# Kernel tuning notes

Hardware: AMD Instinct MI355X
Metric: run time of the kernel (lower is better)

## Reference

```python
import jax, jax.numpy as jnp
import numpy as np

N_USERS = 100000
N_MOVIES = 50000
EMB_DIM = 64
N_EDGES = 5000000


def setup_inputs() -> dict:
    key = jax.random.key(0)
    k1, k2, k3 = jax.random.split(key, 3)
    N = N_USERS + N_MOVIES
    edge_index = jax.random.randint(k1, (2, N_EDGES), 0, N, dtype=jnp.int64)
    user_emb = 0.1 * jax.random.normal(k2, (N_USERS, EMB_DIM), dtype=jnp.float32)
    movie_emb = 0.1 * jax.random.normal(k3, (N_MOVIES, EMB_DIM), dtype=jnp.float32)
    return {"edge_index": edge_index, "n_layers": 3,
            "user_emb": user_emb, "movie_emb": movie_emb}


def reference(edge_index, n_layers, user_emb, movie_emb):
    n_users = user_emb.shape[0]
    N = n_users + movie_emb.shape[0]
    x = jnp.concatenate([user_emb, movie_emb], axis=0)  # [N, D]

    row, col = edge_index[0], edge_index[1]  # source -> target
    # gcn_norm without self-loops (LGConv default): deg from target (col)
    deg = jnp.zeros((N,), x.dtype).at[col].add(1.0)
    dis = jnp.where(deg > 0, jax.lax.rsqrt(jnp.maximum(deg, 1.0)), 0.0)
    norm = dis[row] * dis[col]  # [E]

    acc = x
    total = x
    for _ in range(n_layers):
        msg = acc[row] * norm[:, None]            # [E, D] gather + scale
        acc = jax.ops.segment_sum(msg, col, num_segments=N)  # scatter-add
        total = total + acc
    final = total / (n_layers + 1)                # mean over layers 0..K
    return final[:n_users], final[n_users:]
```

## Files before the change

kernel.cpp:

```cpp
#include <hip/hip_runtime.h>

typedef _Float16 half_t;
typedef _Float16 half2_t __attribute__((ext_vector_type(2)));
union pk_u { unsigned int u; half2_t h; };

#define EMB 64
#define NLAYERS 3
#define BSH2 8
#define BW2 256
#define NB2MAX 1024
#define GSPREAD 32
#define SUBC 8
#define CAP 10240
#define SUBCAP 1280
#define EGCAP 16384
#define P1_BATCH 8192
#define P1_TH 1024
#define P1_EPT 8
#define BINTH 512

__device__ inline int wave_incl_scan(int v) {
    #pragma unroll
    for (int off = 1; off < 64; off <<= 1) {
        int u = __shfl_up(v, off);
        if ((threadIdx.x & 63) >= off) v += u;
    }
    return v;
}

__device__ inline void scan1024(const int* __restrict__ in, int* __restrict__ lstart,
                                int* __restrict__ wsum) {
    int t = threadIdx.x;
    int orig = in[t];
    int v = wave_incl_scan(orig);
    if ((t & 63) == 63) wsum[t >> 6] = v;
    __syncthreads();
    int wid = t >> 6;
    int base = 0;
    #pragma unroll
    for (int w = 0; w < 15; ++w) base += (w < wid) ? wsum[w] : 0;
    lstart[t] = base + v - orig;
    __syncthreads();
}

__device__ inline void scan256(const int* __restrict__ in, int* __restrict__ lstart,
                               int* __restrict__ wsum) {
    int t = threadIdx.x;
    int v = 0, orig = 0;
    if (t < 256) {
        orig = in[t];
        v = wave_incl_scan(orig);
        if ((t & 63) == 63) wsum[t >> 6] = v;
    }
    __syncthreads();
    if (t < 256) {
        int wid = t >> 6;
        int base = 0;
        #pragma unroll
        for (int w = 0; w < 3; ++w) base += (w < wid) ? wsum[w] : 0;
        lstart[t] = base + v - orig;
    }
    __syncthreads();
}

__global__ __launch_bounds__(1024) void part_kernel(
        const int* __restrict__ row, const int* __restrict__ col,
        int* __restrict__ gcount, int* __restrict__ tmp, int E, int nb2) {
    __shared__ int hist[NB2MAX];
    __shared__ int lstart[NB2MAX];
    __shared__ int gbase[NB2MAX];
    __shared__ int wsum[16];
    __shared__ int srec[P1_BATCH];
    __shared__ unsigned short sbuck[P1_BATCH];

    int base = blockIdx.x * P1_BATCH;
    int nE = min(P1_BATCH, E - base);
    int s = blockIdx.x & (SUBC - 1);

    if (threadIdx.x < NB2MAX) hist[threadIdx.x] = 0;
    __syncthreads();

    int myc[P1_EPT];
    #pragma unroll
    for (int k = 0; k < P1_EPT; ++k) {
        int idx = base + (k << 10) + threadIdx.x;
        int c = (idx < E) ? col[idx] : -1;
        myc[k] = c;
        if (c >= 0) atomicAdd(&hist[c >> BSH2], 1);
    }
    __syncthreads();

    scan1024(hist, lstart, wsum);

    if (threadIdx.x < nb2) {
        int b = threadIdx.x;
        int c = hist[b];
        int off = 0;
        if (c > 0) off = atomicAdd(&gcount[(s * NB2MAX + b) * GSPREAD], c);
        gbase[b] = b * CAP + s * SUBCAP + off - lstart[b];
    }
    __syncthreads();
    if (threadIdx.x < NB2MAX) hist[threadIdx.x] = lstart[threadIdx.x];
    __syncthreads();

    #pragma unroll
    for (int k = 0; k < P1_EPT; ++k) {
        int idx = base + (k << 10) + threadIdx.x;
        if (idx < E) {
            int c = myc[k];
            int b = c >> BSH2;
            int r = row[idx];
            int pos = atomicAdd(&hist[b], 1);
            srec[pos] = (r << BSH2) | (c & (BW2 - 1));
            sbuck[pos] = (unsigned short)b;
        }
    }
    __syncthreads();

    if (nE == P1_BATCH) {
        #pragma unroll
        for (int k = 0; k < P1_BATCH / P1_TH; ++k) {
            int i = (k << 10) + threadIdx.x;
            tmp[gbase[sbuck[i]] + i] = srec[i];
        }
    } else {
        for (int i = threadIdx.x; i < nE; i += P1_TH)
            tmp[gbase[sbuck[i]] + i] = srec[i];
    }
}

__global__ __launch_bounds__(512) void bin_kernel(
        const int* __restrict__ tmp, const int* __restrict__ gcount,
        int* __restrict__ eg, int2* __restrict__ sd, float* __restrict__ dis,
        const float4* __restrict__ uev, const float4* __restrict__ mev,
        uint2* __restrict__ s0v, uint2* __restrict__ sbz,
        int n_users, int N) {
    __shared__ int srec[CAP];
    __shared__ int hist[BW2];
    __shared__ int padh[BW2];
    __shared__ int lstart[BW2];
    __shared__ int wsum[4];
    __shared__ float sdis[BW2];
    int b = blockIdx.x;
    int rbase = b * CAP;
    int ebase = b * EGCAP;
    int c0 = b << BSH2;
    int nc = min(BW2, N - c0);
    int sent = N << 7;

    for (int i = threadIdx.x; i < BW2; i += BINTH) hist[i] = 0;
    __syncthreads();

    int cnt = 0;
    #pragma unroll
    for (int ss = 0; ss < SUBC; ++ss) {
        int cs = gcount[(ss * NB2MAX + b) * GSPREAD];
        int sb = rbase + ss * SUBCAP;
        for (int i = threadIdx.x; i < cs; i += BINTH) {
            int rec = tmp[sb + i];
            srec[cnt + i] = rec;
            atomicAdd(&hist[rec & (BW2 - 1)], 1);
        }
        cnt += cs;
    }
    __syncthreads();

    for (int c = threadIdx.x; c < BW2; c += BINTH)
        padh[c] = (hist[c] + 31) & ~31;
    __syncthreads();

    scan256(padh, lstart, wsum);

    for (int c = threadIdx.x; c < nc; c += BINTH) {
        int d = hist[c];
        float dn = (d > 0) ? rsqrtf((float)d) : 0.0f;
        sd[c0 + c] = make_int2(ebase + lstart[c], padh[c]);
        dis[c0 + c] = dn;
        sdis[c] = dn;
    }
    __syncthreads();
    for (int i = threadIdx.x; i < BW2; i += BINTH) hist[i] = lstart[i];
    __syncthreads();

    for (int i = threadIdx.x; i < cnt; i += BINTH) {
        int v = srec[i];
        int pos = atomicAdd(&hist[v & (BW2 - 1)], 1);
        eg[ebase + pos] = (v >> BSH2) << 7;
    }
    __syncthreads();

    for (int i = threadIdx.x; i < BW2 * 32; i += BINTH) {
        int c = i >> 5;
        int o = i & 31;
        int st = hist[c];
        int en = lstart[c] + padh[c];
        if (st + o < en) eg[ebase + st + o] = sent;
    }
    int tot = lstart[BW2 - 1] + padh[BW2 - 1];
    if (threadIdx.x < 64) eg[ebase + tot + threadIdx.x] = sent;

    if (b == 0 && threadIdx.x < 32) {
        int q = threadIdx.x & 15;
        uint2 z = make_uint2(0u, 0u);
        if (threadIdx.x < 16) s0v[(long long)N * 16 + q] = z;
        else                  sbz[(long long)N * 16 + q] = z;
    }

    for (int i = threadIdx.x; i < nc * 16; i += BINTH) {
        int loc = i >> 4;
        int node = c0 + loc;
        int q = i & 15;
        const float4* src = (node < n_users) ? (uev + (long long)node * 16)
                                             : (mev + (long long)(node - n_users) * 16);
        float4 v = src[q];
        float dn = sdis[loc];
        pk_u w0, w1;
        w0.h[0] = (half_t)(v.x * dn); w0.h[1] = (half_t)(v.y * dn);
        w1.h[0] = (half_t)(v.z * dn); w1.h[1] = (half_t)(v.w * dn);
        s0v[(long long)node * 16 + q] = make_uint2(w0.u, w1.u);
    }
}

template <int LAYER>
__global__ __launch_bounds__(256) void gather_kernel(
        const int* __restrict__ eg, const int2* __restrict__ sd,
        const float* __restrict__ dis,
        const uint4* __restrict__ tab, uint2* __restrict__ sOut,
        const uint2* __restrict__ s1v, const uint2* __restrict__ s2v,
        const float4* __restrict__ uev, const float4* __restrict__ mev,
        float4* __restrict__ outv, int n_users, int N) {
    int wave = blockIdx.x * (blockDim.x >> 6) + (threadIdx.x >> 6);
    if (wave >= N) return;
    int l = threadIdx.x & 63;
    int p = l & 7;
    int h = l >> 3;
    unsigned pb = (unsigned)p << 4;
    const char* tb = (const char*)tab;

    int2 se = sd[wave];
    int j = se.x;
    int e = se.x + se.y;
    pk_u a0, a1, a2, a3;
    a0.u = 0; a1.u = 0; a2.u = 0; a3.u = 0;

    if (j < e) {
        int r0 = eg[j + h];
        int r1 = eg[j + 8 + h];
        int r2 = eg[j + 16 + h];
        int r3 = eg[j + 24 + h];
        for (; j < e; j += 32) {
            int n0 = eg[j + 32 + h];
            int n1 = eg[j + 40 + h];
            int n2 = eg[j + 48 + h];
            int n3 = eg[j + 56 + h];
            uint4 v0 = *(const uint4*)(tb + ((unsigned)r0 + pb));
            uint4 v1 = *(const uint4*)(tb + ((unsigned)r1 + pb));
            uint4 v2 = *(const uint4*)(tb + ((unsigned)r2 + pb));
            uint4 v3 = *(const uint4*)(tb + ((unsigned)r3 + pb));
            pk_u t;
            t.u = v0.x; a0.h += t.h; t.u = v0.y; a1.h += t.h;
            t.u = v0.z; a2.h += t.h; t.u = v0.w; a3.h += t.h;
            t.u = v1.x; a0.h += t.h; t.u = v1.y; a1.h += t.h;
            t.u = v1.z; a2.h += t.h; t.u = v1.w; a3.h += t.h;
            t.u = v2.x; a0.h += t.h; t.u = v2.y; a1.h += t.h;
            t.u = v2.z; a2.h += t.h; t.u = v2.w; a3.h += t.h;
            t.u = v3.x; a0.h += t.h; t.u = v3.y; a1.h += t.h;
            t.u = v3.z; a2.h += t.h; t.u = v3.w; a3.h += t.h;
            r0 = n0; r1 = n1; r2 = n2; r3 = n3;
        }
    }

    #pragma unroll
    for (int m = 8; m <= 32; m <<= 1) {
        pk_u t;
        t.u = (unsigned int)__shfl_xor((int)a0.u, m); a0.h += t.h;
        t.u = (unsigned int)__shfl_xor((int)a1.u, m); a1.h += t.h;
        t.u = (unsigned int)__shfl_xor((int)a2.u, m); a2.h += t.h;
        t.u = (unsigned int)__shfl_xor((int)a3.u, m); a3.h += t.h;
    }

    if (h < 2) {
        pk_u x0 = h ? a2 : a0;
        pk_u x1 = h ? a3 : a1;
        float dc = dis[wave];
        float g0 = dc * (float)x0.h[0];
        float g1 = dc * (float)x0.h[1];
        float g2 = dc * (float)x1.h[0];
        float g3 = dc * (float)x1.h[1];
        int q = p * 2 + h;
        long long o16 = (long long)wave * 16 + q;
        if (LAYER < 3) {
            pk_u w0, w1;
            w0.h[0] = (half_t)(dc * g0); w0.h[1] = (half_t)(dc * g1);
            w1.h[0] = (half_t)(dc * g2); w1.h[1] = (half_t)(dc * g3);
            sOut[o16] = make_uint2(w0.u, w1.u);
        } else {
            const float4* src = (wave < n_users) ? (uev + (long long)wave * 16)
                                                 : (mev + (long long)(wave - n_users) * 16);
            float4 xv = src[q];
            float inv = (dc > 0.0f) ? (1.0f / dc) : 0.0f;
            uint2 sa2 = s1v[o16];
            uint2 sb2 = s2v[o16];
            pk_u pa, pb2, pc, pd;
            pa.u = sa2.x; pb2.u = sa2.y; pc.u = sb2.x; pd.u = sb2.y;
            float4 r;
            r.x = (xv.x + ((float)pa.h[0]  + (float)pc.h[0]) * inv + g0) * 0.25f;
            r.y = (xv.y + ((float)pa.h[1]  + (float)pc.h[1]) * inv + g1) * 0.25f;
            r.z = (xv.z + ((float)pb2.h[0] + (float)pd.h[0]) * inv + g2) * 0.25f;
            r.w = (xv.w + ((float)pb2.h[1] + (float)pd.h[1]) * inv + g3) * 0.25f;
            outv[o16] = r;
        }
    }
}

extern "C" void kernel_launch(void* const* d_in, const int* in_sizes, int n_in,
                              void* d_out, int out_size, void* d_ws, size_t ws_size,
                              hipStream_t stream) {
    const int*   edge = (const int*)d_in[0];
    const float* ue   = (const float*)d_in[2];
    const float* me   = (const float*)d_in[3];
    float*       out  = (float*)d_out;

    const int E        = in_sizes[0] / 2;
    const int n_users  = in_sizes[2] / EMB;
    const int n_movies = in_sizes[3] / EMB;
    const int N        = n_users + n_movies;
    const int* row = edge;
    const int* col = edge + E;
    const int nb2 = (N + BW2 - 1) >> BSH2;

    char* ws = (char*)d_ws;
    auto align_up = [](size_t v) { return (v + 255) & ~(size_t)255; };
    int*    gcount = (int*)ws;    ws += align_up((size_t)NB2MAX * SUBC * GSPREAD * sizeof(int));
    int2*   sd     = (int2*)ws;   ws += align_up((size_t)N * sizeof(int2));
    float*  dis    = (float*)ws;  ws += align_up((size_t)N * sizeof(float));
    int*    tmp    = (int*)ws;    ws += align_up((size_t)nb2 * CAP * sizeof(int));
    int*    eg     = (int*)ws;    ws += align_up((size_t)nb2 * EGCAP * sizeof(int));
    half_t* sA     = (half_t*)ws; ws += align_up((size_t)(N + 1) * EMB * sizeof(half_t));
    half_t* sB     = (half_t*)ws; ws += align_up((size_t)(N + 1) * EMB * sizeof(half_t));

    hipMemsetAsync(gcount, 0, (size_t)NB2MAX * SUBC * GSPREAD * sizeof(int), stream);
    part_kernel<<<(E + P1_BATCH - 1) / P1_BATCH, P1_TH, 0, stream>>>(
        row, col, gcount, tmp, E, nb2);
    bin_kernel<<<nb2, BINTH, 0, stream>>>(
        tmp, gcount, eg, sd, dis,
        (const float4*)ue, (const float4*)me, (uint2*)sA, (uint2*)sB,
        n_users, N);

    const int waves_per_block = 4;
    const int gblocks = (N + waves_per_block - 1) / waves_per_block;
    gather_kernel<1><<<gblocks, 256, 0, stream>>>(
        eg, sd, dis, (const uint4*)sA, (uint2*)sB,
        nullptr, nullptr, nullptr, nullptr, nullptr, n_users, N);
    gather_kernel<2><<<gblocks, 256, 0, stream>>>(
        eg, sd, dis, (const uint4*)sB, (uint2*)sA,
        nullptr, nullptr, nullptr, nullptr, nullptr, n_users, N);
    gather_kernel<3><<<gblocks, 256, 0, stream>>>(
        eg, sd, dis, (const uint4*)sA, nullptr,
        (const uint2*)sB, (const uint2*)sA,
        (const float4*)ue, (const float4*)me, (float4*)out, n_users, N);
}
```

Measured before the change: 444.2 us.

## Split bin kernel into two half-bucket blocks and stage edge image in LDS

Each 256-node bucket is now handled by two blocks, each filtering the records for its 128-node half. This doubles grid parallelism and cuts per-block LDS needs. The sorted edge list and its sentinel padding are built in shared memory and then copied out with coalesced int4 stores, replacing scattered global writes. The cost is that every record is read twice across the two blocks. There is also a truncation risk if a half-bucket exceeds SRECMAX or EGIMG.

```diff
diff --git a/kernel.cpp b/kernel.cpp
--- a/kernel.cpp
+++ b/kernel.cpp
@@ -8,12 +8,15 @@
 #define NLAYERS 3
 #define BSH2 8
 #define BW2 256
+#define HB 128
 #define NB2MAX 1024
 #define GSPREAD 32
 #define SUBC 8
 #define CAP 10240
 #define SUBCAP 1280
-#define EGCAP 16384
+#define SRECMAX 5376
+#define EGIMG 9408
+#define EGCAP EGIMG
 #define P1_BATCH 8192
 #define P1_TH 1024
 #define P1_EPT 8
@@ -43,21 +46,18 @@
     __syncthreads();
 }
 
-__device__ inline void scan256(const int* __restrict__ in, int* __restrict__ lstart,
+__device__ inline void scan128(const int* __restrict__ in, int* __restrict__ lstart,
                                int* __restrict__ wsum) {
     int t = threadIdx.x;
     int v = 0, orig = 0;
-    if (t < 256) {
+    if (t < 128) {
         orig = in[t];
         v = wave_incl_scan(orig);
         if ((t & 63) == 63) wsum[t >> 6] = v;
     }
     __syncthreads();
-    if (t < 256) {
-        int wid = t >> 6;
-        int base = 0;
-        #pragma unroll
-        for (int w = 0; w < 3; ++w) base += (w < wid) ? wsum[w] : 0;
+    if (t < 128) {
+        int base = (t >= 64) ? wsum[0] : 0;
         lstart[t] = base + v - orig;
     }
     __syncthreads();
@@ -135,71 +135,87 @@
         const float4* __restrict__ uev, const float4* __restrict__ mev,
         uint2* __restrict__ s0v, uint2* __restrict__ sbz,
         int n_users, int N) {
-    __shared__ int srec[CAP];
-    __shared__ int hist[BW2];
-    __shared__ int padh[BW2];
-    __shared__ int lstart[BW2];
-    __shared__ int wsum[4];
-    __shared__ float sdis[BW2];
-    int b = blockIdx.x;
+    __shared__ alignas(16) int egl[EGIMG];
+    __shared__ int srec[SRECMAX];
+    __shared__ int hist[HB];
+    __shared__ int padh[HB];
+    __shared__ int lstart[HB];
+    __shared__ int curs[HB];
+    __shared__ int wsum[2];
+    __shared__ float sdis[HB];
+    __shared__ int nselS;
+
+    int g = blockIdx.x;
+    int b = g >> 1;
+    int h = g & 1;
     int rbase = b * CAP;
-    int ebase = b * EGCAP;
-    int c0 = b << BSH2;
-    int nc = min(BW2, N - c0);
+    int ebase = g * EGCAP;
+    int c0 = (b << BSH2) + (h << 7);
+    int nc = min(HB, N - c0);
     int sent = N << 7;
 
-    for (int i = threadIdx.x; i < BW2; i += BINTH) hist[i] = 0;
-    __syncthreads();
-
-    int cnt = 0;
+    if (threadIdx.x < HB) hist[threadIdx.x] = 0;
+    if (threadIdx.x == 0) nselS = 0;
+    __syncthreads();
+
     #pragma unroll
     for (int ss = 0; ss < SUBC; ++ss) {
         int cs = gcount[(ss * NB2MAX + b) * GSPREAD];
         int sb = rbase + ss * SUBCAP;
         for (int i = threadIdx.x; i < cs; i += BINTH) {
             int rec = tmp[sb + i];
-            srec[cnt + i] = rec;
-            atomicAdd(&hist[rec & (BW2 - 1)], 1);
-        }
-        cnt += cs;
-    }
-    __syncthreads();
-
-    for (int c = threadIdx.x; c < BW2; c += BINTH)
-        padh[c] = (hist[c] + 31) & ~31;
-    __syncthreads();
-
-    scan256(padh, lstart, wsum);
-
-    for (int c = threadIdx.x; c < nc; c += BINTH) {
-        int d = hist[c];
-        float dn = (d > 0) ? rsqrtf((float)d) : 0.0f;
-        sd[c0 + c] = make_int2(ebase + lstart[c], padh[c]);
-        dis[c0 + c] = dn;
-        sdis[c] = dn;
-    }
-    __syncthreads();
-    for (int i = threadIdx.x; i < BW2; i += BINTH) hist[i] = lstart[i];
-    __syncthreads();
-
-    for (int i = threadIdx.x; i < cnt; i += BINTH) {
+            if (((rec >> 7) & 1) == h) {
+                int pos = atomicAdd(&nselS, 1);
+                if (pos < SRECMAX) srec[pos] = rec;
+                atomicAdd(&hist[rec & (HB - 1)], 1);
+            }
+        }
+    }
+    __syncthreads();
+    int nsel = min(nselS, SRECMAX);
+
+    if (threadIdx.x < HB) padh[threadIdx.x] = (hist[threadIdx.x] + 31) & ~31;
+    __syncthreads();
+
+    scan128(padh, lstart, wsum);
+
+    if (threadIdx.x < HB) {
+        int c = threadIdx.x;
+        if (c < nc) {
+            int d = hist[c];
+            float dn = (d > 0) ? rsqrtf((float)d) : 0.0f;
+            sd[c0 + c] = make_int2(ebase + lstart[c], padh[c]);
+            dis[c0 + c] = dn;
+            sdis[c] = dn;
+        }
+        curs[c] = lstart[c];
+    }
+    __syncthreads();
+
+    for (int i = threadIdx.x; i < nsel; i += BINTH) {
         int v = srec[i];
-        int pos = atomicAdd(&hist[v & (BW2 - 1)], 1);
-        eg[ebase + pos] = (v >> BSH2) << 7;
-    }
-    __syncthreads();
-
-    for (int i = threadIdx.x; i < BW2 * 32; i += BINTH) {
+        int pos = atomicAdd(&curs[v & (HB - 1)], 1);
+        egl[pos] = (v >> 1) & ~127;
+    }
+    __syncthreads();
+
+    for (int i = threadIdx.x; i < HB * 32; i += BINTH) {
         int c = i >> 5;
         int o = i & 31;
-        int st = hist[c];
+        int st = lstart[c] + hist[c];
         int en = lstart[c] + padh[c];
-        if (st + o < en) eg[ebase + st + o] = sent;
-    }
-    int tot = lstart[BW2 - 1] + padh[BW2 - 1];
-    if (threadIdx.x < 64) eg[ebase + tot + threadIdx.x] = sent;
-
-    if (b == 0 && threadIdx.x < 32) {
+        if (st + o < en) egl[st + o] = sent;
+    }
+    int tot = lstart[HB - 1] + padh[HB - 1];
+    if (threadIdx.x < 64) egl[tot + threadIdx.x] = sent;
+    __syncthreads();
+
+    int tw = (tot + 64) >> 2;
+    int4* dst = (int4*)(eg + ebase);
+    const int4* srci = (const int4*)egl;
+    for (int i = threadIdx.x; i < tw; i += BINTH) dst[i] = srci[i];
+
+    if (g == 0 && threadIdx.x < 32) {
         int q = threadIdx.x & 15;
         uint2 z = make_uint2(0u, 0u);
         if (threadIdx.x < 16) s0v[(long long)N * 16 + q] = z;
@@ -335,14 +351,14 @@
     int2*   sd     = (int2*)ws;   ws += align_up((size_t)N * sizeof(int2));
     float*  dis    = (float*)ws;  ws += align_up((size_t)N * sizeof(float));
     int*    tmp    = (int*)ws;    ws += align_up((size_t)nb2 * CAP * sizeof(int));
-    int*    eg     = (int*)ws;    ws += align_up((size_t)nb2 * EGCAP * sizeof(int));
+    int*    eg     = (int*)ws;    ws += align_up((size_t)nb2 * 2 * EGCAP * sizeof(int));
     half_t* sA     = (half_t*)ws; ws += align_up((size_t)(N + 1) * EMB * sizeof(half_t));
     half_t* sB     = (half_t*)ws; ws += align_up((size_t)(N + 1) * EMB * sizeof(half_t));
 
     hipMemsetAsync(gcount, 0, (size_t)NB2MAX * SUBC * GSPREAD * sizeof(int), stream);
     part_kernel<<<(E + P1_BATCH - 1) / P1_BATCH, P1_TH, 0, stream>>>(
         row, col, gcount, tmp, E, nb2);
-    bin_kernel<<<nb2, BINTH, 0, stream>>>(
+    bin_kernel<<<2 * nb2, BINTH, 0, stream>>>(
         tmp, gcount, eg, sd, dis,
         (const float4*)ue, (const float4*)me, (uint2*)sA, (uint2*)sB,
         n_users, N);
```

After: 443.4 us. About the same (-0.2%).

## Replace two-pass bucket partition with global histogram, scan, and atomic scatter CSR build

Applied to the files above, without the earlier changes.

Replaces the bucketed two-level partition (part_kernel plus bin_kernel with shared-memory staging) with a classic CSR build. A per-node global histogram is split over 8 sub-planes, then a two-level prefix scan, a finalize pass that sets offsets, padding and scaled fp16 embeddings, and an atomic scatter of rows into the edge list. This removes the bounded-capacity bucket buffers and the intermediate tmp copy. In exchange it uses global atomics on per-node counters and fully random scatter writes, and the order of edges within a node becomes nondeterministic.

```diff
diff --git a/kernel.cpp b/kernel.cpp
--- a/kernel.cpp
+++ b/kernel.cpp
@@ -6,18 +6,9 @@
 
 #define EMB 64
 #define NLAYERS 3
-#define BSH2 8
-#define BW2 256
-#define NB2MAX 1024
-#define GSPREAD 32
 #define SUBC 8
-#define CAP 10240
-#define SUBCAP 1280
-#define EGCAP 16384
-#define P1_BATCH 8192
-#define P1_TH 1024
-#define P1_EPT 8
-#define BINTH 512
+#define EBLK 8192
+#define NBLK 1024
 
 __device__ inline int wave_incl_scan(int v) {
     #pragma unroll
@@ -28,196 +19,129 @@
     return v;
 }
 
-__device__ inline void scan1024(const int* __restrict__ in, int* __restrict__ lstart,
-                                int* __restrict__ wsum) {
+__global__ __launch_bounds__(1024) void hist_kernel(
+        const int* __restrict__ col, int* __restrict__ cnt2, int E, int NPAD) {
+    int base = blockIdx.x * EBLK;
+    int s = blockIdx.x & (SUBC - 1);
+    int* plane = cnt2 + s * NPAD;
+    #pragma unroll
+    for (int k = 0; k < 8; ++k) {
+        int idx = base + (k << 10) + threadIdx.x;
+        if (idx < E) atomicAdd(&plane[col[idx]], 1);
+    }
+}
+
+__global__ __launch_bounds__(1024) void scanA_kernel(
+        const int* __restrict__ cnt2, int* __restrict__ lstartG,
+        int* __restrict__ bsum, int N, int NPAD) {
+    __shared__ int wsum[16];
+    int node = blockIdx.x * NBLK + threadIdx.x;
+    int pt = 0;
+    if (node < N) {
+        int deg = 0;
+        #pragma unroll
+        for (int s = 0; s < SUBC; ++s) deg += cnt2[s * NPAD + node];
+        pt = (deg + 31) & ~31;
+    }
+    int v = wave_incl_scan(pt);
+    if ((threadIdx.x & 63) == 63) wsum[threadIdx.x >> 6] = v;
+    __syncthreads();
+    int wid = threadIdx.x >> 6;
+    int base = 0;
+    #pragma unroll
+    for (int w = 0; w < 15; ++w) base += (w < wid) ? wsum[w] : 0;
+    if (node < N) lstartG[node] = base + v - pt;
+    if (threadIdx.x == 1023) bsum[blockIdx.x] = base + v;
+}
+
+__global__ __launch_bounds__(1024) void scanB_kernel(
+        const int* __restrict__ bsum, int* __restrict__ bbase,
+        int* __restrict__ totalG, int nb) {
+    __shared__ int wsum[16];
     int t = threadIdx.x;
-    int orig = in[t];
-    int v = wave_incl_scan(orig);
+    int v0 = (t < nb) ? bsum[t] : 0;
+    int v = wave_incl_scan(v0);
     if ((t & 63) == 63) wsum[t >> 6] = v;
     __syncthreads();
     int wid = t >> 6;
     int base = 0;
     #pragma unroll
     for (int w = 0; w < 15; ++w) base += (w < wid) ? wsum[w] : 0;
-    lstart[t] = base + v - orig;
-    __syncthreads();
-}
-
-__device__ inline void scan256(const int* __restrict__ in, int* __restrict__ lstart,
-                               int* __restrict__ wsum) {
-    int t = threadIdx.x;
-    int v = 0, orig = 0;
-    if (t < 256) {
-        orig = in[t];
-        v = wave_incl_scan(orig);
-        if ((t & 63) == 63) wsum[t >> 6] = v;
-    }
-    __syncthreads();
-    if (t < 256) {
-        int wid = t >> 6;
-        int base = 0;
-        #pragma unroll
-        for (int w = 0; w < 3; ++w) base += (w < wid) ? wsum[w] : 0;
-        lstart[t] = base + v - orig;
-    }
-    __syncthreads();
-}
-
-__global__ __launch_bounds__(1024) void part_kernel(
-        const int* __restrict__ row, const int* __restrict__ col,
-        int* __restrict__ gcount, int* __restrict__ tmp, int E, int nb2) {
-    __shared__ int hist[NB2MAX];
-    __shared__ int lstart[NB2MAX];
-    __shared__ int gbase[NB2MAX];
-    __shared__ int wsum[16];
-    __shared__ int srec[P1_BATCH];
-    __shared__ unsigned short sbuck[P1_BATCH];
-
-    int base = blockIdx.x * P1_BATCH;
-    int nE = min(P1_BATCH, E - base);
-    int s = blockIdx.x & (SUBC - 1);
-
-    if (threadIdx.x < NB2MAX) hist[threadIdx.x] = 0;
-    __syncthreads();
-
-    int myc[P1_EPT];
-    #pragma unroll
-    for (int k = 0; k < P1_EPT; ++k) {
-        int idx = base + (k << 10) + threadIdx.x;
-        int c = (idx < E) ? col[idx] : -1;
-        myc[k] = c;
-        if (c >= 0) atomicAdd(&hist[c >> BSH2], 1);
-    }
-    __syncthreads();
-
-    scan1024(hist, lstart, wsum);
-
-    if (threadIdx.x < nb2) {
-        int b = threadIdx.x;
-        int c = hist[b];
-        int off = 0;
-        if (c > 0) off = atomicAdd(&gcount[(s * NB2MAX + b) * GSPREAD], c);
-        gbase[b] = b * CAP + s * SUBCAP + off - lstart[b];
-    }
-    __syncthreads();
-    if (threadIdx.x < NB2MAX) hist[threadIdx.x] = lstart[threadIdx.x];
-    __syncthreads();
-
-    #pragma unroll
-    for (int k = 0; k < P1_EPT; ++k) {
-        int idx = base + (k << 10) + threadIdx.x;
-        if (idx < E) {
-            int c = myc[k];
-            int b = c >> BSH2;
-            int r = row[idx];
-            int pos = atomicAdd(&hist[b], 1);
-            srec[pos] = (r << BSH2) | (c & (BW2 - 1));
-            sbuck[pos] = (unsigned short)b;
-        }
-    }
-    __syncthreads();
-
-    if (nE == P1_BATCH) {
-        #pragma unroll
-        for (int k = 0; k < P1_BATCH / P1_TH; ++k) {
-            int i = (k << 10) + threadIdx.x;
-            tmp[gbase[sbuck[i]] + i] = srec[i];
-        }
-    } else {
-        for (int i = threadIdx.x; i < nE; i += P1_TH)
-            tmp[gbase[sbuck[i]] + i] = srec[i];
-    }
-}
-
-__global__ __launch_bounds__(512) void bin_kernel(
-        const int* __restrict__ tmp, const int* __restrict__ gcount,
+    if (t < nb) bbase[t] = base + v - v0;
+    if (t == 1023) *totalG = base + v;
+}
+
+__global__ __launch_bounds__(1024) void finalize_kernel(
+        int* __restrict__ cnt2, const int* __restrict__ lstartG,
+        const int* __restrict__ bbase, const int* __restrict__ totalG,
         int* __restrict__ eg, int2* __restrict__ sd, float* __restrict__ dis,
         const float4* __restrict__ uev, const float4* __restrict__ mev,
         uint2* __restrict__ s0v, uint2* __restrict__ sbz,
-        int n_users, int N) {
-    __shared__ int srec[CAP];
-    __shared__ int hist[BW2];
-    __shared__ int padh[BW2];
-    __shared__ int lstart[BW2];
-    __shared__ int wsum[4];
-    __shared__ float sdis[BW2];
-    int b = blockIdx.x;
-    int rbase = b * CAP;
-    int ebase = b * EGCAP;
-    int c0 = b << BSH2;
-    int nc = min(BW2, N - c0);
+        int n_users, int N, int NPAD) {
+    __shared__ float sdis[NBLK];
+    int c0 = blockIdx.x * NBLK;
+    int node = c0 + threadIdx.x;
     int sent = N << 7;
 
-    for (int i = threadIdx.x; i < BW2; i += BINTH) hist[i] = 0;
+    if (node < N) {
+        int c[SUBC];
+        int deg = 0;
+        #pragma unroll
+        for (int s = 0; s < SUBC; ++s) { c[s] = cnt2[s * NPAD + node]; deg += c[s]; }
+        int pt = (deg + 31) & ~31;
+        int start = bbase[blockIdx.x] + lstartG[node];
+        float dn = (deg > 0) ? rsqrtf((float)deg) : 0.0f;
+        sd[node] = make_int2(start, pt);
+        dis[node] = dn;
+        sdis[threadIdx.x] = dn;
+        int off = start;
+        #pragma unroll
+        for (int s = 0; s < SUBC; ++s) { int cc = c[s]; cnt2[s * NPAD + node] = off; off += cc; }
+        for (int k = start + deg; k < start + pt; ++k) eg[k] = sent;
+        if (node == N - 1) {
+            int tot = *totalG;
+            for (int k = 0; k < 64; ++k) eg[tot + k] = sent;
+            for (int q = 0; q < 16; ++q) {
+                s0v[(long long)N * 16 + q] = make_uint2(0u, 0u);
+                sbz[(long long)N * 16 + q] = make_uint2(0u, 0u);
+            }
+        }
+    } else {
+        sdis[threadIdx.x] = 0.0f;
+    }
     __syncthreads();
 
-    int cnt = 0;
-    #pragma unroll
-    for (int ss = 0; ss < SUBC; ++ss) {
-        int cs = gcount[(ss * NB2MAX + b) * GSPREAD];
-        int sb = rbase + ss * SUBCAP;
-        for (int i = threadIdx.x; i < cs; i += BINTH) {
-            int rec = tmp[sb + i];
-            srec[cnt + i] = rec;
-            atomicAdd(&hist[rec & (BW2 - 1)], 1);
-        }
-        cnt += cs;
-    }
-    __syncthreads();
-
-    for (int c = threadIdx.x; c < BW2; c += BINTH)
-        padh[c] = (hist[c] + 31) & ~31;
-    __syncthreads();
-
-    scan256(padh, lstart, wsum);
-
-    for (int c = threadIdx.x; c < nc; c += BINTH) {
-        int d = hist[c];
-        float dn = (d > 0) ? rsqrtf((float)d) : 0.0f;
-        sd[c0 + c] = make_int2(ebase + lstart[c], padh[c]);
-        dis[c0 + c] = dn;
-        sdis[c] = dn;
-    }
-    __syncthreads();
-    for (int i = threadIdx.x; i < BW2; i += BINTH) hist[i] = lstart[i];
-    __syncthreads();
-
-    for (int i = threadIdx.x; i < cnt; i += BINTH) {
-        int v = srec[i];
-        int pos = atomicAdd(&hist[v & (BW2 - 1)], 1);
-        eg[ebase + pos] = (v >> BSH2) << 7;
-    }
-    __syncthreads();
-
-    for (int i = threadIdx.x; i < BW2 * 32; i += BINTH) {
-        int c = i >> 5;
-        int o = i & 31;
-        int st = hist[c];
-        int en = lstart[c] + padh[c];
-        if (st + o < en) eg[ebase + st + o] = sent;
-    }
-    int tot = lstart[BW2 - 1] + padh[BW2 - 1];
-    if (threadIdx.x < 64) eg[ebase + tot + threadIdx.x] = sent;
-
-    if (b == 0 && threadIdx.x < 32) {
-        int q = threadIdx.x & 15;
-        uint2 z = make_uint2(0u, 0u);
-        if (threadIdx.x < 16) s0v[(long long)N * 16 + q] = z;
-        else                  sbz[(long long)N * 16 + q] = z;
-    }
-
-    for (int i = threadIdx.x; i < nc * 16; i += BINTH) {
+    int nc = min(NBLK, N - c0);
+    for (int i = threadIdx.x; i < nc * 16; i += NBLK) {
         int loc = i >> 4;
-        int node = c0 + loc;
+        int nd = c0 + loc;
         int q = i & 15;
-        const float4* src = (node < n_users) ? (uev + (long long)node * 16)
-                                             : (mev + (long long)(node - n_users) * 16);
+        const float4* src = (nd < n_users) ? (uev + (long long)nd * 16)
+                                           : (mev + (long long)(nd - n_users) * 16);
         float4 v = src[q];
         float dn = sdis[loc];
         pk_u w0, w1;
         w0.h[0] = (half_t)(v.x * dn); w0.h[1] = (half_t)(v.y * dn);
         w1.h[0] = (half_t)(v.z * dn); w1.h[1] = (half_t)(v.w * dn);
-        s0v[(long long)node * 16 + q] = make_uint2(w0.u, w1.u);
+        s0v[(long long)nd * 16 + q] = make_uint2(w0.u, w1.u);
+    }
+}
+
+__global__ __launch_bounds__(1024) void scatter_kernel(
+        const int* __restrict__ row, const int* __restrict__ col,
+        int* __restrict__ cnt2, int* __restrict__ eg, int E, int NPAD) {
+    int base = blockIdx.x * EBLK;
+    int s = blockIdx.x & (SUBC - 1);
+    int* plane = cnt2 + s * NPAD;
+    #pragma unroll
+    for (int k = 0; k < 8; ++k) {
+        int idx = base + (k << 10) + threadIdx.x;
+        if (idx < E) {
+            int c = col[idx];
+            int r = row[idx];
+            int pos = atomicAdd(&plane[c], 1);
+            eg[pos] = r << 7;
+        }
     }
 }
 
@@ -327,25 +251,32 @@
     const int N        = n_users + n_movies;
     const int* row = edge;
     const int* col = edge + E;
-    const int nb2 = (N + BW2 - 1) >> BSH2;
+    const int NPAD = (N + 63) & ~63;
+    const int eblocks = (E + EBLK - 1) / EBLK;
+    const int nblocks = (N + NBLK - 1) / NBLK;
 
     char* ws = (char*)d_ws;
     auto align_up = [](size_t v) { return (v + 255) & ~(size_t)255; };
-    int*    gcount = (int*)ws;    ws += align_up((size_t)NB2MAX * SUBC * GSPREAD * sizeof(int));
+    int*    cnt2   = (int*)ws;    ws += align_up((size_t)SUBC * NPAD * sizeof(int));
+    int*    lstartG= (int*)ws;    ws += align_up((size_t)N * sizeof(int));
+    int*    bsum   = (int*)ws;    ws += align_up((size_t)1024 * sizeof(int));
+    int*    bbase  = (int*)ws;    ws += align_up((size_t)1024 * sizeof(int));
+    int*    totalG = (int*)ws;    ws += align_up((size_t)64 * sizeof(int));
     int2*   sd     = (int2*)ws;   ws += align_up((size_t)N * sizeof(int2));
     float*  dis    = (float*)ws;  ws += align_up((size_t)N * sizeof(float));
-    int*    tmp    = (int*)ws;    ws += align_up((size_t)nb2 * CAP * sizeof(int));
-    int*    eg     = (int*)ws;    ws += align_up((size_t)nb2 * EGCAP * sizeof(int));
+    int*    eg     = (int*)ws;    ws += align_up(((size_t)E + 31ull * N + 256) * sizeof(int));
     half_t* sA     = (half_t*)ws; ws += align_up((size_t)(N + 1) * EMB * sizeof(half_t));
     half_t* sB     = (half_t*)ws; ws += align_up((size_t)(N + 1) * EMB * sizeof(half_t));
 
-    hipMemsetAsync(gcount, 0, (size_t)NB2MAX * SUBC * GSPREAD * sizeof(int), stream);
-    part_kernel<<<(E + P1_BATCH - 1) / P1_BATCH, P1_TH, 0, stream>>>(
-        row, col, gcount, tmp, E, nb2);
-    bin_kernel<<<nb2, BINTH, 0, stream>>>(
-        tmp, gcount, eg, sd, dis,
+    hipMemsetAsync(cnt2, 0, (size_t)SUBC * NPAD * sizeof(int), stream);
+    hist_kernel<<<eblocks, 1024, 0, stream>>>(col, cnt2, E, NPAD);
+    scanA_kernel<<<nblocks, 1024, 0, stream>>>(cnt2, lstartG, bsum, N, NPAD);
+    scanB_kernel<<<1, 1024, 0, stream>>>(bsum, bbase, totalG, nblocks);
+    finalize_kernel<<<nblocks, 1024, 0, stream>>>(
+        cnt2, lstartG, bbase, totalG, eg, sd, dis,
         (const float4*)ue, (const float4*)me, (uint2*)sA, (uint2*)sB,
-        n_users, N);
+        n_users, N, NPAD);
+    scatter_kernel<<<eblocks, 1024, 0, stream>>>(row, col, cnt2, eg, E, NPAD);
 
     const int waves_per_block = 4;
     const int gblocks = (N + waves_per_block - 1) / waves_per_block;
```

New measurement: 925.2 us. 2.08x slower.
